# Optimization experiments

Hardware: AMD Instinct MI355X
Metric: run time of the kernel (lower is better)

Reference implementation:

```python
import jax, jax.numpy as jnp
from jax import lax
import numpy as np

B, C, H, W = 8, 256, 25, 512
KS = 9
EPS = 1e-5


def setup_inputs() -> dict:
    key = jax.random.key(0)
    ks = jax.random.split(key, 5)
    return {
        "p2_c": jax.random.normal(ks[0], (B, C, H, W), jnp.float32),
        # conv_u_d weight [O,I,9,1]; small scale keeps the 25-step recurrence stable
        "w_msg": jax.random.normal(ks[1], (C, C, KS, 1), jnp.float32) * 0.02,
        "gamma1": jnp.ones((C,), jnp.float32),
        "beta1": jnp.zeros((C,), jnp.float32),
        # conv_up2 adapted to 256->256 (original 64->64 is inconsistent with the data flow)
        "w_up2": jax.random.normal(ks[2], (C, C, 3, 3), jnp.float32) * 0.02,
        "w_conv1": jax.random.normal(ks[3], (1, C, 1, 1), jnp.float32) * 0.05,  # 256->1 1x1
        "w_conv2": jax.random.normal(ks[4], (1, H, 1, 1), jnp.float32) * 0.05,  # 25->1 1x1
    }


def _c_scnn(x, M):
    # x: [B,C,H,W]. Row recurrence: out[0]=x[0]; out[i]=x[i]+relu(M @ out[i-1]).
    # The (9,1) conv on a height-1 slice with pad 4 uses only the center kernel
    # row, i.e. a pure channel-mixing matmul M=[O,I]. Final output is reversed
    # along H exactly as in the original (out[::-1]).
    xs = jnp.moveaxis(x, 2, 0)  # [H,B,C,W]

    def step(prev, xi):
        cur = xi + jax.nn.relu(jnp.einsum('oi,biw->bow', M, prev))
        return cur, cur

    _, rest = lax.scan(step, xs[0], xs[1:])
    outs = jnp.concatenate([xs[:1], rest], axis=0)[::-1]  # reversed rows
    return jnp.moveaxis(outs, 0, 2)  # [B,C,H,W]


def _bn(x, gamma, beta):
    # BatchNorm2d in training mode: per-channel batch stats (biased variance)
    mean = jnp.mean(x, axis=(0, 2, 3), keepdims=True)
    var = jnp.var(x, axis=(0, 2, 3), keepdims=True)
    g = gamma.reshape(1, -1, 1, 1)
    b = beta.reshape(1, -1, 1, 1)
    return g * (x - mean) * lax.rsqrt(var + EPS) + b


def _up_w(x):
    # F.interpolate(size=(H, 2W), mode='bilinear', align_corners=True):
    # height is identity; width is doubled with align_corners mapping.
    w = x.shape[-1]
    wn = 2 * w
    pos = jnp.arange(wn, dtype=x.dtype) * ((w - 1) / (wn - 1))
    i0 = jnp.floor(pos).astype(jnp.int32)
    i1 = jnp.minimum(i0 + 1, w - 1)
    frac = (pos - i0.astype(x.dtype))
    return x[..., i0] * (1.0 - frac) + x[..., i1] * frac


def reference(p2_c, w_msg, gamma1, beta1, w_up2, w_conv1, w_conv2):
    M = w_msg[:, :, KS // 2, 0]  # effective 1x1 channel-mix matrix [O,I]
    x = jax.nn.relu(_bn(_c_scnn(p2_c, M), gamma1, beta1))
    x = jax.nn.relu(_bn(_c_scnn(x, M), gamma1, beta1))
    x = _up_w(x)                                        # [B,256,25,2W]
    x = lax.conv_general_dilated(
        x, w_up2, window_strides=(1, 1), padding=((1, 1), (1, 1)),
        dimension_numbers=('NCHW', 'OIHW', 'NCHW'))     # 3x3 conv
    x = _up_w(x)                                        # [B,256,25,4W]
    x = jnp.einsum('oc,bchw->bohw', w_conv1[:, :, 0, 0], x)  # [B,1,25,4W]
    x = _up_w(x)                                        # [B,1,25,8W]
    x = jnp.transpose(x, (0, 2, 1, 3))                  # [B,25,1,8W]
    x = jnp.einsum('oh,bhcw->bocw', w_conv2[:, :, 0, 0], x)  # [B,1,1,8W]
    return jax.nn.sigmoid(x)
```

## Files before the change

### kernel.cpp

```cpp
#include <hip/hip_runtime.h>
#include <math.h>


#define XBF_OFF    0
#define YBF_OFF    13107200
#define MBF_OFF    26214400
#define COEF1_OFF  26247168
#define COEF2_OFF  26247680
#define WH_OFF     26248192
#define T_OFF      26267392
#define ST1_OFF    26279680
#define ST2_OFF    26280192
#define R_OFF      26280704
#define XIN_OFF    26288896
#define ZERO_FLOATS 13312

typedef __attribute__((ext_vector_type(8))) short bf16x8;
typedef __attribute__((ext_vector_type(4))) float f32x4;

__device__ __forceinline__ ushort f2bf(float f) {
    uint32_t b = __float_as_uint(f);
    b += 0x7fffu + ((b >> 16) & 1u);
    return (ushort)(b >> 16);
}
__device__ __forceinline__ float bf2f(ushort u) {
    return __uint_as_float((uint32_t)u << 16);
}
#define UGET(v, r) ((r) == 0 ? (v).x : (r) == 1 ? (v).y : (r) == 2 ? (v).z : (v).w)

__global__ __launch_bounds__(256) void prep_mbf(const float* __restrict__ wmsg,
                                                ushort* __restrict__ Mbf)
{
    int idx = blockIdx.x * 256 + threadIdx.x;
    Mbf[idx] = f2bf(wmsg[(size_t)idx * 9 + 4]);
}

__global__ __launch_bounds__(256) void prep_wh(const float* __restrict__ wup2,
                                               const float* __restrict__ w1,
                                               const float* __restrict__ w2,
                                               float* __restrict__ wht)
{
    const int c  = blockIdx.x / 3;
    const int kw = blockIdx.x % 3;
    const int o  = threadIdx.x;
    const float w1o = w1[o];
    __shared__ float red[3][256];
    red[0][o] = w1o * wup2[(size_t)((o * 256 + c) * 3 + 0) * 3 + kw];
    red[1][o] = w1o * wup2[(size_t)((o * 256 + c) * 3 + 1) * 3 + kw];
    red[2][o] = w1o * wup2[(size_t)((o * 256 + c) * 3 + 2) * 3 + kw];
    __syncthreads();
    for (int st = 128; st > 0; st >>= 1) {
        if (o < st) {
            red[0][o] += red[0][o + st];
            red[1][o] += red[1][o + st];
            red[2][o] += red[2][o + st];
        }
        __syncthreads();
    }
    if (o < 25) {
        float s = 0.f;
        #pragma unroll
        for (int kh = 0; kh < 3; ++kh) {
            int m = o - kh + 1;
            if (m >= 0 && m < 25) s = fmaf(w2[m], red[kh][0], s);
        }
        wht[(o * 256 + c) * 3 + kw] = s;
    }
}

__global__ __launch_bounds__(256) void xpose(const float* __restrict__ in,
                                             ushort* __restrict__ Xin)
{
    __shared__ float tile[16][520];
    const int tid = threadIdx.x;
    const int bid = blockIdx.x;
    const int b   = bid / 400;
    const int rem = bid - b * 400;
    const int h   = rem >> 4;
    const int cg  = rem & 15;

    #pragma unroll
    for (int k = 0; k < 8; ++k) {
        int f = tid + k * 256;
        int row = f >> 7, col4 = f & 127;
        float4 v = *reinterpret_cast<const float4*>(
            in + ((size_t)((b * 256 + cg * 16 + row) * 25 + h)) * 512 + col4 * 4);
        tile[row][col4 * 4 + 0] = v.x;
        tile[row][col4 * 4 + 1] = v.y;
        tile[row][col4 * 4 + 2] = v.z;
        tile[row][col4 * 4 + 3] = v.w;
    }
    __syncthreads();

    char* outb = (char*)Xin;
    const int wid = cg >> 1, tt = cg & 1;
    #pragma unroll
    for (int k = 0; k < 4; ++k) {
        int s = tid + k * 256;
        int w = s & 511, qq = s >> 9;
        ushort us[8];
        #pragma unroll
        for (int j = 0; j < 8; ++j) us[j] = f2bf(tile[qq * 8 + j][w]);
        size_t dst = ((size_t)(h * 256) + b * 32 + (w >> 4)) * 8192
                   + wid * 1024
                   + ((((tt * 2 + qq) * 256) + (w & 15) * 16) ^ (qq << 5));
        uint4 pk;
        pk.x = (uint)us[0] | ((uint)us[1] << 16);
        pk.y = (uint)us[2] | ((uint)us[3] << 16);
        pk.z = (uint)us[4] | ((uint)us[5] << 16);
        pk.w = (uint)us[6] | ((uint)us[7] << 16);
        *reinterpret_cast<uint4*>(outb + dst) = pk;
    }
}

__global__ __launch_bounds__(512, 2) void scnn_mfma(const ushort* __restrict__ xin_,
                                                    const ushort* __restrict__ Mbf,
                                                    ushort* __restrict__ outf,
                                                    const float* __restrict__ coef,
                                                    float* __restrict__ stats)
{
    __shared__ ulong2 lds_[1024];
    char* lds = (char*)lds_;
    const char* xfr = (const char*)xin_;
    char* ofr = (char*)outf;

    const int tid   = threadIdx.x;
    const int lane  = tid & 63;
    const int wid   = tid >> 6;
    const int row16 = lane & 15;
    const int g     = lane >> 4;
    const int blk   = blockIdx.x;
    const int to0   = wid * 2;

    const int lofs = (lane * 16) ^ (((lane >> 4) & 1) << 5);
    int woff[2];
    #pragma unroll
    for (int tt = 0; tt < 2; ++tt) {
        int inner = (tt * 2 + (g >> 1)) * 256 + row16 * 16 + (g & 1) * 8;
        woff[tt] = wid * 1024 + (inner ^ (((inner >> 8) & 1) << 5));
    }

    bf16x8 afrag[2][8];
    #pragma unroll
    for (int tt = 0; tt < 2; ++tt) {
        const ushort* mrow = Mbf + (size_t)((to0 + tt) * 16 + row16) * 256 + g * 8;
        #pragma unroll
        for (int kk = 0; kk < 8; ++kk)
            afrag[tt][kk] = *reinterpret_cast<const bf16x8*>(mrow + kk * 32);
    }

    const bool hasbn = (coef != nullptr);
    float ca[2][4], cb[2][4];
    if (hasbn) {
        #pragma unroll
        for (int tt = 0; tt < 2; ++tt)
            #pragma unroll
            for (int r = 0; r < 4; ++r) {
                int o = (to0 + tt) * 16 + g * 4 + r;
                ca[tt][r] = coef[o];
                cb[tt][r] = coef[256 + o];
            }
    }

    ushort4 xv4[2], xn4[2];
    #define LDXF(t, dst)                                                       \
        { _Pragma("unroll") for (int tt = 0; tt < 2; ++tt)                     \
              dst[tt] = *reinterpret_cast<const ushort4*>(                     \
                  xfr + ((size_t)(t) * 256 + blk) * 8192 + woff[tt]); }

    LDXF(0, xv4);
    LDXF(1, xn4);

    float s1[2][4] = {{0,0,0,0},{0,0,0,0}};
    float sq[2][4] = {{0,0,0,0},{0,0,0,0}};

    for (int t = 0; t < 25; ++t) {
        ushort4 x24[2];
        if (t < 23) LDXF(t + 2, x24);

        f32x4 acc[2] = {{0.f,0.f,0.f,0.f},{0.f,0.f,0.f,0.f}};
        if (t > 0) {
            const char* pb = lds + (t & 1) * 8192 + lofs;
            #pragma unroll
            for (int kk = 0; kk < 8; ++kk) {
                bf16x8 bfr = *reinterpret_cast<const bf16x8*>(pb + kk * 1024);
                acc[0] = __builtin_amdgcn_mfma_f32_16x16x32_bf16(afrag[0][kk], bfr, acc[0], 0, 0, 0);
                acc[1] = __builtin_amdgcn_mfma_f32_16x16x32_bf16(afrag[1][kk], bfr, acc[1], 0, 0, 0);
            }
        }

        char* wb = lds + ((t & 1) ^ 1) * 8192;
        char* ob = ofr + ((size_t)(24 - t) * 256 + blk) * 8192;
        #pragma unroll
        for (int tt = 0; tt < 2; ++tt) {
            ushort us[4];
            #pragma unroll
            for (int r = 0; r < 4; ++r) {
                float x = bf2f(UGET(xv4[tt], r));
                if (hasbn) x = fmaxf(fmaf(ca[tt][r], x, cb[tt][r]), 0.0f);
                float cv = x + fmaxf(acc[tt][r], 0.0f);
                us[r] = f2bf(cv);
                s1[tt][r] += cv;
                sq[tt][r] = fmaf(cv, cv, sq[tt][r]);
            }
            ushort4 u4 = make_ushort4(us[0], us[1], us[2], us[3]);
            *reinterpret_cast<ushort4*>(ob + woff[tt]) = u4;
            *reinterpret_cast<ushort4*>(wb + woff[tt]) = u4;
        }

        if (t < 24) {
            asm volatile("s_waitcnt lgkmcnt(0)" ::: "memory");
            __builtin_amdgcn_s_barrier();
            __builtin_amdgcn_sched_barrier(0);
        }

        #pragma unroll
        for (int tt = 0; tt < 2; ++tt) { xv4[tt] = xn4[tt]; xn4[tt] = x24[tt]; }
    }

    #pragma unroll
    for (int tt = 0; tt < 2; ++tt)
        #pragma unroll
        for (int r = 0; r < 4; ++r) {
            float a = s1[tt][r], q2 = sq[tt][r];
            #pragma unroll
            for (int m = 8; m >= 1; m >>= 1) {
                a  += __shfl_xor(a, m, 64);
                q2 += __shfl_xor(q2, m, 64);
            }
            if (row16 == 0) {
                int o = (to0 + tt) * 16 + g * 4 + r;
                atomicAdd(&stats[o], a);
                atomicAdd(&stats[256 + o], q2);
            }
        }
}

__global__ __launch_bounds__(256) void coef_kernel(const float* __restrict__ stats,
                                                   const float* __restrict__ gamma,
                                                   const float* __restrict__ beta,
                                                   float* __restrict__ coef)
{
    int c = threadIdx.x;
    float mean = stats[c] * (1.0f / 102400.0f);
    float var  = stats[256 + c] * (1.0f / 102400.0f) - mean * mean;
    float a = gamma[c] * rsqrtf(var + 1e-5f);
    coef[c] = a;
    coef[256 + c] = beta[c] - mean * a;
}

__global__ __launch_bounds__(512) void conv_reduce(const ushort* __restrict__ Yf_,
                                                   const float* __restrict__ coef2,
                                                   const float* __restrict__ wht,
                                                   float* __restrict__ T)
{
    const char* Yf = (const char*)Yf_;
    const int tid   = threadIdx.x;
    const int lane  = tid & 63;
    const int wid   = tid >> 6;
    const int row16 = lane & 15;
    const int g     = lane >> 4;
    const int blk   = blockIdx.x;
    const int b     = blk >> 5;
    const int w0    = (blk & 31) << 4;
    const int to0   = wid * 2;

    int woff[2], ch0[2];
    #pragma unroll
    for (int tt = 0; tt < 2; ++tt) {
        int inner = (tt * 2 + (g >> 1)) * 256 + row16 * 16 + (g & 1) * 8;
        woff[tt] = wid * 1024 + (inner ^ (((inner >> 8) & 1) << 5));
        ch0[tt]  = (to0 + tt) * 16 + g * 4;
    }

    float a2[2][4], b2[2][4];
    #pragma unroll
    for (int tt = 0; tt < 2; ++tt)
        #pragma unroll
        for (int r = 0; r < 4; ++r) {
            a2[tt][r] = coef2[ch0[tt] + r];
            b2[tt][r] = coef2[256 + ch0[tt] + r];
        }

    float acc0 = 0.f, acc1 = 0.f, acc2 = 0.f;
    for (int h = 0; h < 25; ++h) {
        #pragma unroll
        for (int tt = 0; tt < 2; ++tt) {
            ushort4 y4 = *reinterpret_cast<const ushort4*>(
                Yf + ((size_t)h * 256 + blk) * 8192 + woff[tt]);
            const float* wb = wht + ((size_t)h * 256 + ch0[tt]) * 3;
            float4 qa = *reinterpret_cast<const float4*>(wb);
            float4 qb = *reinterpret_cast<const float4*>(wb + 4);
            float4 qc = *reinterpret_cast<const float4*>(wb + 8);
            float A[12] = {qa.x, qa.y, qa.z, qa.w, qb.x, qb.y,
                           qb.z, qb.w, qc.x, qc.y, qc.z, qc.w};
            #pragma unroll
            for (int r = 0; r < 4; ++r) {
                float z = fmaxf(fmaf(a2[tt][r], bf2f(UGET(y4, r)), b2[tt][r]), 0.f);
                acc0 = fmaf(A[r * 3 + 0], z, acc0);
                acc1 = fmaf(A[r * 3 + 1], z, acc1);
                acc2 = fmaf(A[r * 3 + 2], z, acc2);
            }
        }
    }

    acc0 += __shfl_xor(acc0, 16, 64); acc0 += __shfl_xor(acc0, 32, 64);
    acc1 += __shfl_xor(acc1, 16, 64); acc1 += __shfl_xor(acc1, 32, 64);
    acc2 += __shfl_xor(acc2, 16, 64); acc2 += __shfl_xor(acc2, 32, 64);

    __shared__ float red[8][3][16];
    if (lane < 16) {
        red[wid][0][lane] = acc0;
        red[wid][1][lane] = acc1;
        red[wid][2][lane] = acc2;
    }
    __syncthreads();
    if (tid < 48) {
        int kw = tid >> 4, col = tid & 15;
        float s = 0.f;
        #pragma unroll
        for (int w8 = 0; w8 < 8; ++w8) s += red[w8][kw][col];
        T[(size_t)(kw * 8 + b) * 512 + w0 + col] = s;
    }
}

__global__ __launch_bounds__(256) void combine_r(const float* __restrict__ T,
                                                 float* __restrict__ r)
{
    int idx = blockIdx.x * 256 + threadIdx.x;
    int b = idx >> 10, w = idx & 1023;
    const float scale = (float)(511.0 / 1023.0);
    float acc = 0.f;
    #pragma unroll
    for (int kw = 0; kw < 3; ++kw) {
        int u = w + kw - 1;
        if (u >= 0 && u < 1024) {
            float pos = (float)u * scale;
            int i0 = (int)pos;
            float f = pos - (float)i0;
            int i1 = min(i0 + 1, 511);
            const float* Tk = T + (size_t)(kw * 8 + b) * 512;
            float lo = Tk[i0];
            acc += fmaf(Tk[i1] - lo, f, lo);
        }
    }
    r[idx] = acc;
}

__global__ __launch_bounds__(256) void final_kernel(const float* __restrict__ r,
                                                    float* __restrict__ out)
{
    int idx = blockIdx.x * 256 + threadIdx.x;
    int b = idx >> 12, w4 = idx & 4095;
    const float s3 = (float)(2047.0 / 4095.0);
    const float s2 = (float)(1023.0 / 2047.0);
    const float* rb = r + b * 1024;

    float pos3 = (float)w4 * s3;
    int j0 = (int)pos3;
    float f3 = pos3 - (float)j0;
    int j1 = min(j0 + 1, 2047);

    float v[2];
    int jj[2] = {j0, j1};
    #pragma unroll
    for (int k = 0; k < 2; ++k) {
        float p = (float)jj[k] * s2;
        int i = (int)p;
        float f = p - (float)i;
        int i2 = min(i + 1, 1023);
        float lo = rb[i];
        v[k] = fmaf(rb[i2] - lo, f, lo);
    }
    float z = fmaf(v[1] - v[0], f3, v[0]);
    out[idx] = 1.0f / (1.0f + expf(-z));
}

extern "C" void kernel_launch(void* const* d_in, const int* in_sizes, int n_in,
                              void* d_out, int out_size, void* d_ws, size_t ws_size,
                              hipStream_t stream)
{
    const float* p2c   = (const float*)d_in[0];
    const float* wmsg  = (const float*)d_in[1];
    const float* gamma = (const float*)d_in[2];
    const float* beta  = (const float*)d_in[3];
    const float* wup2  = (const float*)d_in[4];
    const float* wc1   = (const float*)d_in[5];
    const float* wc2   = (const float*)d_in[6];
    float* out = (float*)d_out;
    float* ws  = (float*)d_ws;

    ushort* Xf    = (ushort*)(ws + XBF_OFF);
    ushort* Yf    = (ushort*)(ws + YBF_OFF);
    ushort* Mbf   = (ushort*)(ws + MBF_OFF);
    float*  coef1 = ws + COEF1_OFF;
    float*  coef2 = ws + COEF2_OFF;
    float*  wht   = ws + WH_OFF;
    float*  T     = ws + T_OFF;
    float*  st1   = ws + ST1_OFF;
    float*  st2   = ws + ST2_OFF;
    float*  r     = ws + R_OFF;
    ushort* Xin   = (ushort*)(ws + XIN_OFF);

    hipMemsetAsync(T, 0, ZERO_FLOATS * sizeof(float), stream);

    prep_mbf<<<256, 256, 0, stream>>>(wmsg, Mbf);
    prep_wh<<<768, 256, 0, stream>>>(wup2, wc1, wc2, wht);

    xpose<<<3200, 256, 0, stream>>>(p2c, Xin);

    scnn_mfma<<<256, 512, 0, stream>>>(Xin, Mbf, Xf, nullptr, st1);
    coef_kernel<<<1, 256, 0, stream>>>(st1, gamma, beta, coef1);

    scnn_mfma<<<256, 512, 0, stream>>>(Xf, Mbf, Yf, coef1, st2);
    coef_kernel<<<1, 256, 0, stream>>>(st2, gamma, beta, coef2);

    conv_reduce<<<256, 512, 0, stream>>>(Yf, coef2, wht, T);
    combine_r<<<32, 256, 0, stream>>>(T, r);

    final_kernel<<<128, 256, 0, stream>>>(r, out);
}
```

Measured before the change: 165.0 us.

## Split SCNN recurrence across 16 waves per block and replace memset with stats-zero kernel

The row-recurrence kernel now runs with 1024 threads per block, so each wave computes a single 16-channel output tile instead of two. This halves the serial MFMA chain and per-step epilogue work each wave does between barriers. The cost is twice as many waves joining every per-step barrier, and a launch bound that allows only one block per CU. Separately, the hipMemsetAsync over the accumulation buffers is replaced by a small kernel that zeroes only the BN stats region. That relies on the later reduction no longer needing a pre-zeroed T buffer.

```diff
diff --git a/kernel.cpp b/kernel.cpp
--- a/kernel.cpp
+++ b/kernel.cpp
@@ -13,7 +13,6 @@
 #define ST2_OFF    26280192
 #define R_OFF      26280704
 #define XIN_OFF    26288896
-#define ZERO_FLOATS 13312
 
 typedef __attribute__((ext_vector_type(8))) short bf16x8;
 typedef __attribute__((ext_vector_type(4))) float f32x4;
@@ -68,6 +67,11 @@
     }
 }
 
+__global__ __launch_bounds__(256) void zero_st(float* __restrict__ st)
+{
+    st[blockIdx.x * 256 + threadIdx.x] = 0.f;
+}
+
 __global__ __launch_bounds__(256) void xpose(const float* __restrict__ in,
                                              ushort* __restrict__ Xin)
 {
@@ -113,11 +117,11 @@
     }
 }
 
-__global__ __launch_bounds__(512, 2) void scnn_mfma(const ushort* __restrict__ xin_,
-                                                    const ushort* __restrict__ Mbf,
-                                                    ushort* __restrict__ outf,
-                                                    const float* __restrict__ coef,
-                                                    float* __restrict__ stats)
+__global__ __launch_bounds__(1024, 1) void scnn_mfma(const ushort* __restrict__ xin_,
+                                                     const ushort* __restrict__ Mbf,
+                                                     ushort* __restrict__ outf,
+                                                     const float* __restrict__ coef,
+                                                     float* __restrict__ stats)
 {
     __shared__ ulong2 lds_[1024];
     char* lds = (char*)lds_;
@@ -130,83 +134,69 @@
     const int row16 = lane & 15;
     const int g     = lane >> 4;
     const int blk   = blockIdx.x;
-    const int to0   = wid * 2;
 
     const int lofs = (lane * 16) ^ (((lane >> 4) & 1) << 5);
-    int woff[2];
-    #pragma unroll
-    for (int tt = 0; tt < 2; ++tt) {
-        int inner = (tt * 2 + (g >> 1)) * 256 + row16 * 16 + (g & 1) * 8;
-        woff[tt] = wid * 1024 + (inner ^ (((inner >> 8) & 1) << 5));
-    }
-
-    bf16x8 afrag[2][8];
-    #pragma unroll
-    for (int tt = 0; tt < 2; ++tt) {
-        const ushort* mrow = Mbf + (size_t)((to0 + tt) * 16 + row16) * 256 + g * 8;
+    int inner = (((wid & 1) * 2 + (g >> 1)) * 256) + row16 * 16 + (g & 1) * 8;
+    const int woff = (wid >> 1) * 1024 + (inner ^ (((inner >> 8) & 1) << 5));
+
+    bf16x8 afrag[8];
+    {
+        const ushort* mrow = Mbf + (size_t)(wid * 16 + row16) * 256 + g * 8;
         #pragma unroll
         for (int kk = 0; kk < 8; ++kk)
-            afrag[tt][kk] = *reinterpret_cast<const bf16x8*>(mrow + kk * 32);
+            afrag[kk] = *reinterpret_cast<const bf16x8*>(mrow + kk * 32);
     }
 
     const bool hasbn = (coef != nullptr);
-    float ca[2][4], cb[2][4];
+    float ca[4], cb[4];
     if (hasbn) {
         #pragma unroll
-        for (int tt = 0; tt < 2; ++tt)
-            #pragma unroll
-            for (int r = 0; r < 4; ++r) {
-                int o = (to0 + tt) * 16 + g * 4 + r;
-                ca[tt][r] = coef[o];
-                cb[tt][r] = coef[256 + o];
-            }
-    }
-
-    ushort4 xv4[2], xn4[2];
-    #define LDXF(t, dst)                                                       \
-        { _Pragma("unroll") for (int tt = 0; tt < 2; ++tt)                     \
-              dst[tt] = *reinterpret_cast<const ushort4*>(                     \
-                  xfr + ((size_t)(t) * 256 + blk) * 8192 + woff[tt]); }
-
-    LDXF(0, xv4);
-    LDXF(1, xn4);
-
-    float s1[2][4] = {{0,0,0,0},{0,0,0,0}};
-    float sq[2][4] = {{0,0,0,0},{0,0,0,0}};
+        for (int r = 0; r < 4; ++r) {
+            int o = wid * 16 + g * 4 + r;
+            ca[r] = coef[o];
+            cb[r] = coef[256 + o];
+        }
+    }
+
+    ushort4 xv4, xn4;
+    #define LDXF(t) (*reinterpret_cast<const ushort4*>(                        \
+        xfr + ((size_t)(t) * 256 + blk) * 8192 + woff))
+
+    xv4 = LDXF(0);
+    xn4 = LDXF(1);
+
+    float s1[4] = {0, 0, 0, 0};
+    float sq[4] = {0, 0, 0, 0};
 
     for (int t = 0; t < 25; ++t) {
-        ushort4 x24[2];
-        if (t < 23) LDXF(t + 2, x24);
-
-        f32x4 acc[2] = {{0.f,0.f,0.f,0.f},{0.f,0.f,0.f,0.f}};
+        ushort4 x24;
+        if (t < 23) x24 = LDXF(t + 2);
+
+        f32x4 acc = {0.f, 0.f, 0.f, 0.f};
         if (t > 0) {
             const char* pb = lds + (t & 1) * 8192 + lofs;
             #pragma unroll
             for (int kk = 0; kk < 8; ++kk) {
                 bf16x8 bfr = *reinterpret_cast<const bf16x8*>(pb + kk * 1024);
-                acc[0] = __builtin_amdgcn_mfma_f32_16x16x32_bf16(afrag[0][kk], bfr, acc[0], 0, 0, 0);
-                acc[1] = __builtin_amdgcn_mfma_f32_16x16x32_bf16(afrag[1][kk], bfr, acc[1], 0, 0, 0);
+                acc = __builtin_amdgcn_mfma_f32_16x16x32_bf16(afrag[kk], bfr, acc, 0, 0, 0);
             }
         }
 
         char* wb = lds + ((t & 1) ^ 1) * 8192;
         char* ob = ofr + ((size_t)(24 - t) * 256 + blk) * 8192;
-        #pragma unroll
-        for (int tt = 0; tt < 2; ++tt) {
-            ushort us[4];
-            #pragma unroll
-            for (int r = 0; r < 4; ++r) {
-                float x = bf2f(UGET(xv4[tt], r));
-                if (hasbn) x = fmaxf(fmaf(ca[tt][r], x, cb[tt][r]), 0.0f);
-                float cv = x + fmaxf(acc[tt][r], 0.0f);
-                us[r] = f2bf(cv);
-                s1[tt][r] += cv;
-                sq[tt][r] = fmaf(cv, cv, sq[tt][r]);
-            }
-            ushort4 u4 = make_ushort4(us[0], us[1], us[2], us[3]);
-            *reinterpret_cast<ushort4*>(ob + woff[tt]) = u4;
-            *reinterpret_cast<ushort4*>(wb + woff[tt]) = u4;
-        }
+        ushort us[4];
+        #pragma unroll
+        for (int r = 0; r < 4; ++r) {
+            float x = bf2f(UGET(xv4, r));
+            if (hasbn) x = fmaxf(fmaf(ca[r], x, cb[r]), 0.0f);
+            float cv = x + fmaxf(acc[r], 0.0f);
+            us[r] = f2bf(cv);
+            s1[r] += cv;
+            sq[r] = fmaf(cv, cv, sq[r]);
+        }
+        ushort4 u4 = make_ushort4(us[0], us[1], us[2], us[3]);
+        *reinterpret_cast<ushort4*>(ob + woff) = u4;
+        *reinterpret_cast<ushort4*>(wb + woff) = u4;
 
         if (t < 24) {
             asm volatile("s_waitcnt lgkmcnt(0)" ::: "memory");
@@ -214,26 +204,23 @@
             __builtin_amdgcn_sched_barrier(0);
         }
 
-        #pragma unroll
-        for (int tt = 0; tt < 2; ++tt) { xv4[tt] = xn4[tt]; xn4[tt] = x24[tt]; }
-    }
-
-    #pragma unroll
-    for (int tt = 0; tt < 2; ++tt)
-        #pragma unroll
-        for (int r = 0; r < 4; ++r) {
-            float a = s1[tt][r], q2 = sq[tt][r];
-            #pragma unroll
-            for (int m = 8; m >= 1; m >>= 1) {
-                a  += __shfl_xor(a, m, 64);
-                q2 += __shfl_xor(q2, m, 64);
-            }
-            if (row16 == 0) {
-                int o = (to0 + tt) * 16 + g * 4 + r;
-                atomicAdd(&stats[o], a);
-                atomicAdd(&stats[256 + o], q2);
-            }
-        }
+        xv4 = xn4; xn4 = x24;
+    }
+
+    #pragma unroll
+    for (int r = 0; r < 4; ++r) {
+        float a = s1[r], q2 = sq[r];
+        #pragma unroll
+        for (int m = 8; m >= 1; m >>= 1) {
+            a  += __shfl_xor(a, m, 64);
+            q2 += __shfl_xor(q2, m, 64);
+        }
+        if (row16 == 0) {
+            int o = wid * 16 + g * 4 + r;
+            atomicAdd(&stats[o], a);
+            atomicAdd(&stats[256 + o], q2);
+        }
+    }
 }
 
 __global__ __launch_bounds__(256) void coef_kernel(const float* __restrict__ stats,
@@ -402,17 +389,17 @@
     float*  r     = ws + R_OFF;
     ushort* Xin   = (ushort*)(ws + XIN_OFF);
 
-    hipMemsetAsync(T, 0, ZERO_FLOATS * sizeof(float), stream);
+    zero_st<<<4, 256, 0, stream>>>(st1);
 
     prep_mbf<<<256, 256, 0, stream>>>(wmsg, Mbf);
     prep_wh<<<768, 256, 0, stream>>>(wup2, wc1, wc2, wht);
 
     xpose<<<3200, 256, 0, stream>>>(p2c, Xin);
 
-    scnn_mfma<<<256, 512, 0, stream>>>(Xin, Mbf, Xf, nullptr, st1);
+    scnn_mfma<<<256, 1024, 0, stream>>>(Xin, Mbf, Xf, nullptr, st1);
     coef_kernel<<<1, 256, 0, stream>>>(st1, gamma, beta, coef1);
 
-    scnn_mfma<<<256, 512, 0, stream>>>(Xf, Mbf, Yf, coef1, st2);
+    scnn_mfma<<<256, 1024, 0, stream>>>(Xf, Mbf, Yf, coef1, st2);
     coef_kernel<<<1, 256, 0, stream>>>(st2, gamma, beta, coef2);
 
     conv_reduce<<<256, 512, 0, stream>>>(Yf, coef2, wht, T);
```

After: 163.9 us. Within noise of the previous version (-0.7%).

## Stage recurrence inputs via async global-to-LDS DMA and widen transpose tiles

Applied to the files above, without the earlier changes.

The SCNN recurrence kernel now prefetches each row's input tile into a triple-buffered LDS staging area with global_load_lds and explicit vmcnt waits, instead of holding register prefetches. It writes outputs with inline dwordx2 stores and drops the occupancy hint to one block per CU. The transpose kernel handles 32 channels per block with a new write pattern, halving its grid. The memset is replaced by a small kernel that zeroes only the BN stats buffers, which risks leaving T uninitialised if conv_reduce accumulates into it.

```diff
diff --git a/kernel.cpp b/kernel.cpp
--- a/kernel.cpp
+++ b/kernel.cpp
@@ -13,7 +13,6 @@
 #define ST2_OFF    26280192
 #define R_OFF      26280704
 #define XIN_OFF    26288896
-#define ZERO_FLOATS 13312
 
 typedef __attribute__((ext_vector_type(8))) short bf16x8;
 typedef __attribute__((ext_vector_type(4))) float f32x4;
@@ -27,6 +26,17 @@
     return __uint_as_float((uint32_t)u << 16);
 }
 #define UGET(v, r) ((r) == 0 ? (v).x : (r) == 1 ? (v).y : (r) == 2 ? (v).z : (v).w)
+
+__device__ __forceinline__ void dma16(const void* g, void* l) {
+    __builtin_amdgcn_global_load_lds(
+        (const __attribute__((address_space(1))) uint32_t*)g,
+        (__attribute__((address_space(3))) uint32_t*)l, 16, 0, 0);
+}
+__device__ __forceinline__ void store8(void* p, uint lo, uint hi) {
+    uint64_t addr = (uint64_t)(uintptr_t)p;
+    uint64_t val  = (uint64_t)lo | ((uint64_t)hi << 32);
+    asm volatile("global_store_dwordx2 %0, %1, off" :: "v"(addr), "v"(val) : "memory");
+}
 
 __global__ __launch_bounds__(256) void prep_mbf(const float* __restrict__ wmsg,
                                                 ushort* __restrict__ Mbf)
@@ -68,23 +78,28 @@
     }
 }
 
+__global__ __launch_bounds__(256) void zero_st(float* __restrict__ st)
+{
+    st[blockIdx.x * 256 + threadIdx.x] = 0.f;
+}
+
 __global__ __launch_bounds__(256) void xpose(const float* __restrict__ in,
                                              ushort* __restrict__ Xin)
 {
-    __shared__ float tile[16][520];
+    __shared__ float tile[32][522];
     const int tid = threadIdx.x;
     const int bid = blockIdx.x;
-    const int b   = bid / 400;
-    const int rem = bid - b * 400;
-    const int h   = rem >> 4;
-    const int cg  = rem & 15;
-
-    #pragma unroll
-    for (int k = 0; k < 8; ++k) {
+    const int b   = bid / 200;
+    const int rem = bid - b * 200;
+    const int h   = rem >> 3;
+    const int wg  = rem & 7;
+
+    #pragma unroll
+    for (int k = 0; k < 16; ++k) {
         int f = tid + k * 256;
         int row = f >> 7, col4 = f & 127;
         float4 v = *reinterpret_cast<const float4*>(
-            in + ((size_t)((b * 256 + cg * 16 + row) * 25 + h)) * 512 + col4 * 4);
+            in + ((size_t)((b * 256 + wg * 32 + row) * 25 + h)) * 512 + col4 * 4);
         tile[row][col4 * 4 + 0] = v.x;
         tile[row][col4 * 4 + 1] = v.y;
         tile[row][col4 * 4 + 2] = v.z;
@@ -93,17 +108,19 @@
     __syncthreads();
 
     char* outb = (char*)Xin;
-    const int wid = cg >> 1, tt = cg & 1;
-    #pragma unroll
-    for (int k = 0; k < 4; ++k) {
-        int s = tid + k * 256;
-        int w = s & 511, qq = s >> 9;
+    const int wv   = tid >> 6;
+    const int lane = tid & 63;
+    const int qq   = lane >> 4, wcol = lane & 15;
+    int inner = qq * 256 + wcol * 16;
+    inner ^= ((inner >> 8) & 1) << 5;
+    #pragma unroll
+    for (int j = 0; j < 8; ++j) {
+        int w16 = wv * 8 + j;
+        int w = w16 * 16 + wcol;
         ushort us[8];
         #pragma unroll
-        for (int j = 0; j < 8; ++j) us[j] = f2bf(tile[qq * 8 + j][w]);
-        size_t dst = ((size_t)(h * 256) + b * 32 + (w >> 4)) * 8192
-                   + wid * 1024
-                   + ((((tt * 2 + qq) * 256) + (w & 15) * 16) ^ (qq << 5));
+        for (int i = 0; i < 8; ++i) us[i] = f2bf(tile[qq * 8 + i][w]);
+        size_t dst = ((size_t)(h * 256) + b * 32 + w16) * 8192 + wg * 1024 + inner;
         uint4 pk;
         pk.x = (uint)us[0] | ((uint)us[1] << 16);
         pk.y = (uint)us[2] | ((uint)us[3] << 16);
@@ -113,14 +130,16 @@
     }
 }
 
-__global__ __launch_bounds__(512, 2) void scnn_mfma(const ushort* __restrict__ xin_,
+__global__ __launch_bounds__(512, 1) void scnn_mfma(const ushort* __restrict__ xin_,
                                                     const ushort* __restrict__ Mbf,
                                                     ushort* __restrict__ outf,
                                                     const float* __restrict__ coef,
                                                     float* __restrict__ stats)
 {
-    __shared__ ulong2 lds_[1024];
-    char* lds = (char*)lds_;
+    __shared__ ulong2 state_[1024];
+    __shared__ ulong2 xst_[1536];
+    char* lds = (char*)state_;
+    char* xst = (char*)xst_;
     const char* xfr = (const char*)xin_;
     char* ofr = (char*)outf;
 
@@ -139,6 +158,7 @@
         int inner = (tt * 2 + (g >> 1)) * 256 + row16 * 16 + (g & 1) * 8;
         woff[tt] = wid * 1024 + (inner ^ (((inner >> 8) & 1) << 5));
     }
+    const int dofs = tid * 16;
 
     bf16x8 afrag[2][8];
     #pragma unroll
@@ -162,21 +182,33 @@
             }
     }
 
-    ushort4 xv4[2], xn4[2];
-    #define LDXF(t, dst)                                                       \
-        { _Pragma("unroll") for (int tt = 0; tt < 2; ++tt)                     \
-              dst[tt] = *reinterpret_cast<const ushort4*>(                     \
-                  xfr + ((size_t)(t) * 256 + blk) * 8192 + woff[tt]); }
-
-    LDXF(0, xv4);
-    LDXF(1, xn4);
+    #define DMA(t, sbuf) dma16(xfr + ((size_t)(t) * 256 + blk) * 8192 + dofs,  \
+                               xst + (sbuf) * 8192 + dofs)
+
+    DMA(0, 0);
+    DMA(1, 1);
+    __builtin_amdgcn_sched_barrier(0);
 
     float s1[2][4] = {{0,0,0,0},{0,0,0,0}};
     float sq[2][4] = {{0,0,0,0},{0,0,0,0}};
 
+    int sb = 0;
     for (int t = 0; t < 25; ++t) {
-        ushort4 x24[2];
-        if (t < 23) LDXF(t + 2, x24);
+        if (t == 0)      asm volatile("s_waitcnt vmcnt(1)" ::: "memory");
+        else if (t == 1) asm volatile("s_waitcnt vmcnt(3)" ::: "memory");
+        else             asm volatile("s_waitcnt vmcnt(5)" ::: "memory");
+        __builtin_amdgcn_sched_barrier(0);
+
+        ushort4 xv4[2];
+        #pragma unroll
+        for (int tt = 0; tt < 2; ++tt)
+            xv4[tt] = *reinterpret_cast<const ushort4*>(xst + sb * 8192 + woff[tt]);
+
+        if (t < 23) {
+            int nb = sb + 2; if (nb >= 3) nb -= 3;
+            DMA(t + 2, nb);
+        }
+        __builtin_amdgcn_sched_barrier(0);
 
         f32x4 acc[2] = {{0.f,0.f,0.f,0.f},{0.f,0.f,0.f,0.f}};
         if (t > 0) {
@@ -203,9 +235,10 @@
                 s1[tt][r] += cv;
                 sq[tt][r] = fmaf(cv, cv, sq[tt][r]);
             }
-            ushort4 u4 = make_ushort4(us[0], us[1], us[2], us[3]);
-            *reinterpret_cast<ushort4*>(ob + woff[tt]) = u4;
-            *reinterpret_cast<ushort4*>(wb + woff[tt]) = u4;
+            uint lo = (uint)us[0] | ((uint)us[1] << 16);
+            uint hi = (uint)us[2] | ((uint)us[3] << 16);
+            store8(ob + woff[tt], lo, hi);
+            *reinterpret_cast<uint2*>(wb + woff[tt]) = make_uint2(lo, hi);
         }
 
         if (t < 24) {
@@ -213,9 +246,7 @@
             __builtin_amdgcn_s_barrier();
             __builtin_amdgcn_sched_barrier(0);
         }
-
-        #pragma unroll
-        for (int tt = 0; tt < 2; ++tt) { xv4[tt] = xn4[tt]; xn4[tt] = x24[tt]; }
+        sb = (sb == 2) ? 0 : sb + 1;
     }
 
     #pragma unroll
@@ -402,12 +433,12 @@
     float*  r     = ws + R_OFF;
     ushort* Xin   = (ushort*)(ws + XIN_OFF);
 
-    hipMemsetAsync(T, 0, ZERO_FLOATS * sizeof(float), stream);
+    zero_st<<<4, 256, 0, stream>>>(st1);
 
     prep_mbf<<<256, 256, 0, stream>>>(wmsg, Mbf);
     prep_wh<<<768, 256, 0, stream>>>(wup2, wc1, wc2, wht);
 
-    xpose<<<3200, 256, 0, stream>>>(p2c, Xin);
+    xpose<<<1600, 256, 0, stream>>>(p2c, Xin);
 
     scnn_mfma<<<256, 512, 0, stream>>>(Xin, Mbf, Xf, nullptr, st1);
     coef_kernel<<<1, 256, 0, stream>>>(st1, gamma, beta, coef1);
```

New measurement: 165.5 us. No clear change (+0.3%).

## Split SCNN recurrence into 8-column blocks to double grid size

Applied to the files above, without the earlier changes.

Repacks the bf16 activation layout so each scnn_mfma and conv_reduce block covers 8 width columns instead of 16, and launches 512 blocks instead of 256. The xpose kernel is reorganised to match, and the host memset is replaced with a small kernel that zeroes only the BN stat buffers. The goal is to spread the serial 25-step recurrence over more workgroups so the machine is better filled. In exchange, half of each 16-wide MFMA tile now does redundant work, since the upper lanes are masked out of stores and reductions. Total MFMA work doubles, and two blocks may compete for the same CU.

```diff
diff --git a/kernel.cpp b/kernel.cpp
--- a/kernel.cpp
+++ b/kernel.cpp
@@ -13,7 +13,6 @@
 #define ST2_OFF    26280192
 #define R_OFF      26280704
 #define XIN_OFF    26288896
-#define ZERO_FLOATS 13312
 
 typedef __attribute__((ext_vector_type(8))) short bf16x8;
 typedef __attribute__((ext_vector_type(4))) float f32x4;
@@ -68,23 +67,28 @@
     }
 }
 
+__global__ __launch_bounds__(256) void zero_st(float* __restrict__ st)
+{
+    st[blockIdx.x * 256 + threadIdx.x] = 0.f;
+}
+
 __global__ __launch_bounds__(256) void xpose(const float* __restrict__ in,
                                              ushort* __restrict__ Xin)
 {
-    __shared__ float tile[16][520];
+    __shared__ float tile[32][522];
     const int tid = threadIdx.x;
     const int bid = blockIdx.x;
-    const int b   = bid / 400;
-    const int rem = bid - b * 400;
-    const int h   = rem >> 4;
-    const int cg  = rem & 15;
-
-    #pragma unroll
-    for (int k = 0; k < 8; ++k) {
+    const int b   = bid / 200;
+    const int rem = bid - b * 200;
+    const int h   = rem >> 3;
+    const int wg  = rem & 7;
+
+    #pragma unroll
+    for (int k = 0; k < 16; ++k) {
         int f = tid + k * 256;
         int row = f >> 7, col4 = f & 127;
         float4 v = *reinterpret_cast<const float4*>(
-            in + ((size_t)((b * 256 + cg * 16 + row) * 25 + h)) * 512 + col4 * 4);
+            in + ((size_t)((b * 256 + wg * 32 + row) * 25 + h)) * 512 + col4 * 4);
         tile[row][col4 * 4 + 0] = v.x;
         tile[row][col4 * 4 + 1] = v.y;
         tile[row][col4 * 4 + 2] = v.z;
@@ -93,17 +97,17 @@
     __syncthreads();
 
     char* outb = (char*)Xin;
-    const int wid = cg >> 1, tt = cg & 1;
-    #pragma unroll
-    for (int k = 0; k < 4; ++k) {
-        int s = tid + k * 256;
-        int w = s & 511, qq = s >> 9;
+    const int idx  = tid & 31;
+    const int gp   = idx >> 3, wcol = idx & 7;
+    const int wsub = tid >> 5;
+    #pragma unroll
+    for (int it = 0; it < 8; ++it) {
+        int w8 = it * 8 + wsub;
+        int w  = w8 * 8 + wcol;
         ushort us[8];
         #pragma unroll
-        for (int j = 0; j < 8; ++j) us[j] = f2bf(tile[qq * 8 + j][w]);
-        size_t dst = ((size_t)(h * 256) + b * 32 + (w >> 4)) * 8192
-                   + wid * 1024
-                   + ((((tt * 2 + qq) * 256) + (w & 15) * 16) ^ (qq << 5));
+        for (int j = 0; j < 8; ++j) us[j] = f2bf(tile[gp * 8 + j][w]);
+        size_t dst = ((size_t)h * 512 + b * 64 + w8) * 4096 + wg * 512 + idx * 16;
         uint4 pk;
         pk.x = (uint)us[0] | ((uint)us[1] << 16);
         pk.y = (uint)us[2] | ((uint)us[3] << 16);
@@ -119,8 +123,8 @@
                                                     const float* __restrict__ coef,
                                                     float* __restrict__ stats)
 {
-    __shared__ ulong2 lds_[1024];
-    char* lds = (char*)lds_;
+    __shared__ ulong2 state_[512];
+    char* lds = (char*)state_;
     const char* xfr = (const char*)xin_;
     char* ofr = (char*)outf;
 
@@ -128,17 +132,17 @@
     const int lane  = tid & 63;
     const int wid   = tid >> 6;
     const int row16 = lane & 15;
+    const int wcol  = row16 & 7;
+    const bool live = (row16 < 8);
     const int g     = lane >> 4;
     const int blk   = blockIdx.x;
     const int to0   = wid * 2;
 
-    const int lofs = (lane * 16) ^ (((lane >> 4) & 1) << 5);
+    const int lofs = (g * 8 + wcol) * 16;
     int woff[2];
     #pragma unroll
-    for (int tt = 0; tt < 2; ++tt) {
-        int inner = (tt * 2 + (g >> 1)) * 256 + row16 * 16 + (g & 1) * 8;
-        woff[tt] = wid * 1024 + (inner ^ (((inner >> 8) & 1) << 5));
-    }
+    for (int tt = 0; tt < 2; ++tt)
+        woff[tt] = wid * 512 + (tt * 2 + (g >> 1)) * 128 + wcol * 16 + (g & 1) * 8;
 
     bf16x8 afrag[2][8];
     #pragma unroll
@@ -166,7 +170,7 @@
     #define LDXF(t, dst)                                                       \
         { _Pragma("unroll") for (int tt = 0; tt < 2; ++tt)                     \
               dst[tt] = *reinterpret_cast<const ushort4*>(                     \
-                  xfr + ((size_t)(t) * 256 + blk) * 8192 + woff[tt]); }
+                  xfr + ((size_t)(t) * 512 + blk) * 4096 + woff[tt]); }
 
     LDXF(0, xv4);
     LDXF(1, xn4);
@@ -180,17 +184,17 @@
 
         f32x4 acc[2] = {{0.f,0.f,0.f,0.f},{0.f,0.f,0.f,0.f}};
         if (t > 0) {
-            const char* pb = lds + (t & 1) * 8192 + lofs;
+            const char* pb = lds + (t & 1) * 4096 + lofs;
             #pragma unroll
             for (int kk = 0; kk < 8; ++kk) {
-                bf16x8 bfr = *reinterpret_cast<const bf16x8*>(pb + kk * 1024);
+                bf16x8 bfr = *reinterpret_cast<const bf16x8*>(pb + kk * 512);
                 acc[0] = __builtin_amdgcn_mfma_f32_16x16x32_bf16(afrag[0][kk], bfr, acc[0], 0, 0, 0);
                 acc[1] = __builtin_amdgcn_mfma_f32_16x16x32_bf16(afrag[1][kk], bfr, acc[1], 0, 0, 0);
             }
         }
 
-        char* wb = lds + ((t & 1) ^ 1) * 8192;
-        char* ob = ofr + ((size_t)(24 - t) * 256 + blk) * 8192;
+        char* wb = lds + ((t & 1) ^ 1) * 4096;
+        char* ob = ofr + ((size_t)(24 - t) * 512 + blk) * 4096;
         #pragma unroll
         for (int tt = 0; tt < 2; ++tt) {
             ushort us[4];
@@ -203,9 +207,11 @@
                 s1[tt][r] += cv;
                 sq[tt][r] = fmaf(cv, cv, sq[tt][r]);
             }
-            ushort4 u4 = make_ushort4(us[0], us[1], us[2], us[3]);
-            *reinterpret_cast<ushort4*>(ob + woff[tt]) = u4;
-            *reinterpret_cast<ushort4*>(wb + woff[tt]) = u4;
+            uint lo = (uint)us[0] | ((uint)us[1] << 16);
+            uint hi = (uint)us[2] | ((uint)us[3] << 16);
+            *reinterpret_cast<uint2*>(wb + woff[tt]) = make_uint2(lo, hi);
+            if (live)
+                *reinterpret_cast<uint2*>(ob + woff[tt]) = make_uint2(lo, hi);
         }
 
         if (t < 24) {
@@ -224,7 +230,7 @@
         for (int r = 0; r < 4; ++r) {
             float a = s1[tt][r], q2 = sq[tt][r];
             #pragma unroll
-            for (int m = 8; m >= 1; m >>= 1) {
+            for (int m = 4; m >= 1; m >>= 1) {
                 a  += __shfl_xor(a, m, 64);
                 q2 += __shfl_xor(q2, m, 64);
             }
@@ -259,18 +265,18 @@
     const int lane  = tid & 63;
     const int wid   = tid >> 6;
     const int row16 = lane & 15;
+    const int wcol  = row16 & 7;
+    const float mask = (row16 < 8) ? 1.f : 0.f;
     const int g     = lane >> 4;
     const int blk   = blockIdx.x;
-    const int b     = blk >> 5;
-    const int w0    = (blk & 31) << 4;
-    const int to0   = wid * 2;
+    const int b     = blk >> 6;
+    const int w0    = (blk & 63) << 3;
 
     int woff[2], ch0[2];
     #pragma unroll
     for (int tt = 0; tt < 2; ++tt) {
-        int inner = (tt * 2 + (g >> 1)) * 256 + row16 * 16 + (g & 1) * 8;
-        woff[tt] = wid * 1024 + (inner ^ (((inner >> 8) & 1) << 5));
-        ch0[tt]  = (to0 + tt) * 16 + g * 4;
+        woff[tt] = wid * 512 + (tt * 2 + (g >> 1)) * 128 + wcol * 16 + (g & 1) * 8;
+        ch0[tt]  = wid * 32 + tt * 16 + g * 4;
     }
 
     float a2[2][4], b2[2][4];
@@ -287,7 +293,7 @@
         #pragma unroll
         for (int tt = 0; tt < 2; ++tt) {
             ushort4 y4 = *reinterpret_cast<const ushort4*>(
-                Yf + ((size_t)h * 256 + blk) * 8192 + woff[tt]);
+                Yf + ((size_t)h * 512 + blk) * 4096 + woff[tt]);
             const float* wb = wht + ((size_t)h * 256 + ch0[tt]) * 3;
             float4 qa = *reinterpret_cast<const float4*>(wb);
             float4 qb = *reinterpret_cast<const float4*>(wb + 4);
@@ -303,20 +309,21 @@
             }
         }
     }
+    acc0 *= mask; acc1 *= mask; acc2 *= mask;
 
     acc0 += __shfl_xor(acc0, 16, 64); acc0 += __shfl_xor(acc0, 32, 64);
     acc1 += __shfl_xor(acc1, 16, 64); acc1 += __shfl_xor(acc1, 32, 64);
     acc2 += __shfl_xor(acc2, 16, 64); acc2 += __shfl_xor(acc2, 32, 64);
 
-    __shared__ float red[8][3][16];
-    if (lane < 16) {
+    __shared__ float red[8][3][8];
+    if (lane < 8) {
         red[wid][0][lane] = acc0;
         red[wid][1][lane] = acc1;
         red[wid][2][lane] = acc2;
     }
     __syncthreads();
-    if (tid < 48) {
-        int kw = tid >> 4, col = tid & 15;
+    if (tid < 24) {
+        int kw = tid >> 3, col = tid & 7;
         float s = 0.f;
         #pragma unroll
         for (int w8 = 0; w8 < 8; ++w8) s += red[w8][kw][col];
@@ -402,20 +409,20 @@
     float*  r     = ws + R_OFF;
     ushort* Xin   = (ushort*)(ws + XIN_OFF);
 
-    hipMemsetAsync(T, 0, ZERO_FLOATS * sizeof(float), stream);
+    zero_st<<<4, 256, 0, stream>>>(st1);
 
     prep_mbf<<<256, 256, 0, stream>>>(wmsg, Mbf);
     prep_wh<<<768, 256, 0, stream>>>(wup2, wc1, wc2, wht);
 
-    xpose<<<3200, 256, 0, stream>>>(p2c, Xin);
-
-    scnn_mfma<<<256, 512, 0, stream>>>(Xin, Mbf, Xf, nullptr, st1);
+    xpose<<<1600, 256, 0, stream>>>(p2c, Xin);
+
+    scnn_mfma<<<512, 512, 0, stream>>>(Xin, Mbf, Xf, nullptr, st1);
     coef_kernel<<<1, 256, 0, stream>>>(st1, gamma, beta, coef1);
 
-    scnn_mfma<<<256, 512, 0, stream>>>(Xf, Mbf, Yf, coef1, st2);
+    scnn_mfma<<<512, 512, 0, stream>>>(Xf, Mbf, Yf, coef1, st2);
     coef_kernel<<<1, 256, 0, stream>>>(st2, gamma, beta, coef2);
 
-    conv_reduce<<<256, 512, 0, stream>>>(Yf, coef2, wht, T);
+    conv_reduce<<<512, 512, 0, stream>>>(Yf, coef2, wht, T);
     combine_r<<<32, 256, 0, stream>>>(T, r);
 
     final_kernel<<<128, 256, 0, stream>>>(r, out);
```

Measured after the change: 241.6 us. 1.46x slower.
